# Kernel tuning notes

Hardware: AMD Instinct MI355X
Metric: run time of the kernel (lower is better)

Reference implementation:

```python
import jax, jax.numpy as jnp
import numpy as np

N_NODES = 50000
N_EDGES = 500000
N_GRAPHS = 1024
NF = 128          # node_feature
DIST_DIM = 64
SH_DIM = 64
SH_IN = 9         # spherical_harmonics_l**2, l=3
IN_DIM = 92
N_LAYERS = 5
RBF_BINS = 64
RBF_VMIN, RBF_VMAX = 0.125, 1.4


def _lin(x, W, b):
    return x @ W + b


def setup_inputs() -> dict:
    key = jax.random.key(0)
    ks = jax.random.split(key, 32)
    s = lambda fan_in: 1.0 / np.sqrt(fan_in)

    def W(k, i, o):
        return jax.random.uniform(k, (i, o), jnp.float32, -s(i), s(i))

    inp = {
        "x": jax.random.normal(ks[0], (N_NODES, IN_DIM), jnp.float32),
        "edge_index": jax.random.randint(ks[1], (2, N_EDGES), 0, N_NODES, jnp.int64),
        "sh": jax.random.normal(ks[2], (N_EDGES, SH_IN), jnp.float32),
        "edge_dist": jax.random.uniform(ks[3], (N_EDGES,), jnp.float32, 0.2, 1.0),
        "batch": jnp.sort(jax.random.randint(ks[4], (N_NODES,), 0, N_GRAPHS, jnp.int64)),
        # atom embedding
        "W_emb": W(ks[5], IN_DIM, NF), "b_emb": jnp.zeros((NF,), jnp.float32),
        # sh_mlp: 9 -> 32 -> 64
        "sh_W1": W(ks[6], SH_IN, 32), "sh_b1": jnp.zeros((32,), jnp.float32),
        "sh_W2": W(ks[7], 32, SH_DIM), "sh_b2": jnp.zeros((SH_DIM,), jnp.float32),
        # rbf tail: 64 -> 64 -> 64
        "rbf_W1": W(ks[8], RBF_BINS, 64), "rbf_b1": jnp.zeros((64,), jnp.float32),
        "rbf_W2": W(ks[9], 64, DIST_DIM), "rbf_b2": jnp.zeros((DIST_DIM,), jnp.float32),
        # SFTConv (CGConv-style gated message) stacked over layers: z dim = 3*NF
        "Wg": jnp.stack([W(jax.random.fold_in(ks[10], l), 3 * NF, NF) for l in range(N_LAYERS)]),
        "bg": jnp.zeros((N_LAYERS, NF), jnp.float32),
        "Wc": jnp.stack([W(jax.random.fold_in(ks[11], l), 3 * NF, NF) for l in range(N_LAYERS)]),
        "bc": jnp.zeros((N_LAYERS, NF), jnp.float32),
        # readout fc: 128 -> 128 -> 1
        "fc_W1": W(ks[12], NF, 128), "fc_b1": jnp.zeros((128,), jnp.float32),
        "fc_W2": W(ks[13], 128, 1), "fc_b2": jnp.zeros((1,), jnp.float32),
    }
    return inp


def reference(x, edge_index, sh, edge_dist, batch,
              W_emb, b_emb, sh_W1, sh_b1, sh_W2, sh_b2,
              rbf_W1, rbf_b1, rbf_W2, rbf_b2,
              Wg, bg, Wc, bc, fc_W1, fc_b1, fc_W2, fc_b2):
    # atom embedding: [N, 92] -> [N, 128]
    h = _lin(x, W_emb, b_emb)

    # spherical harmonics edge MLP: [E, 9] -> [E, 64]
    sh_e = _lin(jax.nn.silu(_lin(sh, sh_W1, sh_b1)), sh_W2, sh_b2)

    # RBF expansion of inverse distance (no_grad in torch -> stop_gradient)
    inv_d = jax.lax.stop_gradient(1.0 / edge_dist)[:, None]       # [E, 1]
    centers = jnp.linspace(RBF_VMIN, RBF_VMAX, RBF_BINS, dtype=jnp.float32)
    gamma = 1.0 / (centers[1] - centers[0]) ** 2
    rbf = jnp.exp(-gamma * (inv_d - centers) ** 2)                # [E, 64]
    dist_e = _lin(jax.nn.silu(_lin(rbf, rbf_W1, rbf_b1)), rbf_W2, rbf_b2)

    edge_attr = jnp.concatenate([dist_e, sh_e], axis=-1)          # [E, 128]

    src, dst = edge_index[0], edge_index[1]
    n_nodes = h.shape[0]
    for l in range(Wg.shape[0]):
        # gated CGConv-style message: z = [h_dst, h_src, e]  -> [E, 384]
        z = jnp.concatenate([h[dst], h[src], edge_attr], axis=-1)
        m = jax.nn.sigmoid(z @ Wg[l] + bg[l]) * jax.nn.softplus(z @ Wc[l] + bc[l])
        agg = jax.ops.segment_sum(m, dst, num_segments=n_nodes)   # [N, 128]
        h = h + agg

    # scatter-mean readout over batch ids
    sums = jax.ops.segment_sum(h, batch, num_segments=N_GRAPHS)   # [G, 128]
    counts = jax.ops.segment_sum(jnp.ones((n_nodes,), h.dtype), batch, num_segments=N_GRAPHS)
    pooled = sums / jnp.maximum(counts, 1.0)[:, None]

    out = _lin(jax.nn.silu(_lin(pooled, fc_W1, fc_b1)), fc_W2, fc_b2)  # [G, 1]
    return out.squeeze(-1)
```

## Files before the change

### kernel.cpp

```cpp
#include <hip/hip_runtime.h>

typedef __bf16 bf16x8 __attribute__((ext_vector_type(8)));
typedef __bf16 bf16x4 __attribute__((ext_vector_type(4)));
typedef float  f32x4  __attribute__((ext_vector_type(4)));

#define N_NODES  50000
#define N_EDGES  500000
#define EB       128
#define EP       500096
#define NCH      12
#define N_GRAPHS 1024
#define NF       128
#define IN_DIM   92
#define N_LAYERS 5
#define SPANMAX  256

__device__ __forceinline__ float sigmoidf_(float x) { return 1.0f / (1.0f + __expf(-x)); }
__device__ __forceinline__ float softplusf_(float x) {
    return fmaxf(x, 0.0f) + __logf(1.0f + __expf(-fabsf(x)));
}
__device__ __forceinline__ float siluf_(float x) { return x * sigmoidf_(x); }

__global__ void __launch_bounds__(256) k_fold(const float* __restrict__ Wg,
    const float* __restrict__ Wc, const float* __restrict__ rbW2,
    const float* __restrict__ rbB2, const float* __restrict__ shW2,
    const float* __restrict__ shB2, const float* __restrict__ bg,
    const float* __restrict__ bc, float* __restrict__ Wfold,
    float* __restrict__ bF) {
    int lg = blockIdx.x, l = lg >> 1, g = lg & 1;
    const float* W = (g ? Wc : Wg) + (size_t)l * 384 * 128;
    const float* bsrc = (g ? bc : bg) + l * 128;
    int tid = threadIdx.x;
    for (int idx = tid; idx < 96 * 128; idx += 256) {
        int r = idx >> 7, n = idx & 127;
        float s = 0.f;
        if (r < 64) {
            for (int o = 0; o < 64; ++o) s += rbW2[r * 64 + o] * W[(256 + o) * 128 + n];
        } else {
            int j = r - 64;
            for (int o = 0; o < 64; ++o) s += shW2[j * 64 + o] * W[(320 + o) * 128 + n];
        }
        Wfold[(size_t)lg * 12288 + idx] = s;
    }
    if (tid < 128) {
        float s = bsrc[tid];
        for (int o = 0; o < 64; ++o) s += rbB2[o] * W[(256 + o) * 128 + tid];
        for (int o = 0; o < 64; ++o) s += shB2[o] * W[(320 + o) * 128 + tid];
        bF[lg * 128 + tid] = s;
    }
}

__global__ void __launch_bounds__(256) k_prep_w(const float* __restrict__ Wg,
                                                const float* __restrict__ Wc,
                                                const float* __restrict__ Wfold,
                                                __bf16* __restrict__ WeT,
                                                __bf16* __restrict__ WnT) {
    int t = blockIdx.x * 256 + threadIdx.x;
    if (t >= (240 + 640) * 64) return;
    int frag = t >> 6, lane = t & 63;
    int sub = lane >> 4, mm = lane & 15;
    bf16x8 v;
    if (frag < 240) {
        int lg = frag / 24; int r = frag % 24;
        int m = r / 3; int ks = r % 3;
        #pragma unroll
        for (int j = 0; j < 8; ++j) {
            int k = ks * 32 + sub * 8 + j;
            v[j] = (__bf16)Wfold[(size_t)lg * 12288 + (size_t)k * 128 + m * 16 + mm];
        }
        *(bf16x8*)(WeT + (size_t)frag * 512 + lane * 8) = v;
    } else {
        int f2 = frag - 240;
        int l = f2 / 128; int r = f2 % 128;
        int m = r >> 2; int ks = r & 3;
        int F = m * 16 + mm;
        #pragma unroll
        for (int j = 0; j < 8; ++j) {
            int k = ks * 32 + sub * 8 + j;
            float val;
            if      (F < 128) val = Wg[(size_t)l*384*128 + (size_t)k*128 + F];
            else if (F < 256) val = Wc[(size_t)l*384*128 + (size_t)k*128 + (F-128)];
            else if (F < 384) val = Wg[(size_t)l*384*128 + (size_t)(128+k)*128 + (F-256)];
            else              val = Wc[(size_t)l*384*128 + (size_t)(128+k)*128 + (F-384)];
            v[j] = (__bf16)val;
        }
        *(bf16x8*)(WnT + (size_t)f2 * 512 + lane * 8) = v;
    }
}

__global__ void __launch_bounds__(256) k_deg(const int* __restrict__ dstI,
                                             int* __restrict__ deg) {
    int e = blockIdx.x * 256 + threadIdx.x;
    if (e < N_EDGES) atomicAdd(&deg[dstI[e]], 1);
}

__global__ void __launch_bounds__(1024) k_scan(const int* __restrict__ deg,
                                               int* __restrict__ cursor) {
    __shared__ int ps[1024];
    int t = threadIdx.x;
    const int C = (N_NODES + 1023) / 1024;
    int base = t * C;
    int s = 0;
    for (int i = 0; i < C; ++i) { int idx = base + i; if (idx < N_NODES) s += deg[idx]; }
    ps[t] = s;
    __syncthreads();
    for (int off = 1; off < 1024; off <<= 1) {
        int v = 0;
        if (t >= off) v = ps[t - off];
        __syncthreads();
        if (t >= off) ps[t] += v;
        __syncthreads();
    }
    int run = (t > 0) ? ps[t - 1] : 0;
    for (int i = 0; i < C; ++i) {
        int idx = base + i;
        if (idx < N_NODES) { cursor[idx] = run; run += deg[idx]; }
    }
}

__global__ void __launch_bounds__(256) k_scatter(const int* __restrict__ srcI,
                                                 const int* __restrict__ dstI,
                                                 int* __restrict__ cursor,
                                                 int* __restrict__ perm,
                                                 int* __restrict__ dstS,
                                                 int2* __restrict__ sdS) {
    int e = blockIdx.x * 256 + threadIdx.x;
    if (e >= N_EDGES) return;
    int d = dstI[e];
    int p = atomicAdd(&cursor[d], 1);
    perm[p] = e;
    dstS[p] = d;
    sdS[p] = make_int2(d, srcI[e]);
}

__global__ void __launch_bounds__(128) k_pad(int* __restrict__ dstS,
                                             int2* __restrict__ sdS,
                                             char* __restrict__ ea2) {
    int i = threadIdx.x;
    if (i < EP - N_EDGES) {
        dstS[N_EDGES + i] = N_NODES;
        sdS[N_EDGES + i] = make_int2(N_NODES, 0);
        uint4 z = {0, 0, 0, 0};
        for (int p = 0; p < NCH; ++p)
            *(uint4*)(ea2 + ((size_t)p * EP + N_EDGES + i) * 16) = z;
    }
}

__global__ void __launch_bounds__(256) k_embed(const float* __restrict__ x,
                                               const float* __restrict__ W,
                                               const float* __restrict__ b,
                                               float* __restrict__ h) {
    int tid = threadIdx.x;
    int f = tid & 127;
    int nb = blockIdx.x * 8 + (tid >> 7) * 4;
    const float* x0 = x + (size_t)nb * IN_DIM;
    float a0 = b[f], a1 = a0, a2 = a0, a3 = a0;
    #pragma unroll 4
    for (int k = 0; k < IN_DIM; ++k) {
        float wv = W[k * NF + f];
        a0 = fmaf(x0[k], wv, a0);
        a1 = fmaf(x0[IN_DIM + k], wv, a1);
        a2 = fmaf(x0[2 * IN_DIM + k], wv, a2);
        a3 = fmaf(x0[3 * IN_DIM + k], wv, a3);
    }
    float accs[4] = {a0, a1, a2, a3};
    #pragma unroll
    for (int r = 0; r < 4; ++r)
        h[(size_t)(nb + r) * NF + f] = accs[r];
}

__global__ void __launch_bounds__(256) k_edge(const float* __restrict__ sh,
    const float* __restrict__ dist, const int* __restrict__ perm,
    const float* __restrict__ shW1, const float* __restrict__ shB1,
    const float* __restrict__ rbW1, const float* __restrict__ rbB1,
    char* __restrict__ ea2) {
    __shared__ float wf[4480];
    int tid = threadIdx.x;
    int p = blockIdx.x * 256 + tid;
    bool pv = p < N_EDGES;
    int e = pv ? perm[p] : 0;
    float dv = dist[e];
    float shv[9];
    #pragma unroll
    for (int i = 0; i < 9; ++i) shv[i] = sh[(size_t)e * 9 + i];
    for (int i = tid; i < 288;  i += 256) wf[i]        = shW1[i];
    for (int i = tid; i < 32;   i += 256) wf[288 + i]  = shB1[i];
    for (int i = tid; i < 4096; i += 256) wf[320 + i]  = rbW1[i];
    for (int i = tid; i < 64;   i += 256) wf[4416 + i] = rbB1[i];
    __syncthreads();
    if (!pv) return;

    const float* W1 = wf + 320; const float* B1 = wf + 4416;
    float invd = 1.0f / dv;
    const float step = (1.4f - 0.125f) / 63.0f;
    const float gam = 1.0f / (step * step);
    float hid[64];
    #pragma unroll
    for (int j = 0; j < 64; ++j) hid[j] = B1[j];
    for (int i = 0; i < 64; ++i) {
        float c = 0.125f + i * step;
        float d = invd - c;
        float r = __expf(-gam * d * d);
        #pragma unroll
        for (int j = 0; j < 64; ++j) hid[j] += r * W1[i * 64 + j];
    }
    #pragma unroll
    for (int o8 = 0; o8 < 8; ++o8) {
        bf16x8 v;
        #pragma unroll
        for (int j = 0; j < 8; ++j) v[j] = (__bf16)siluf_(hid[o8 * 8 + j]);
        *(bf16x8*)(ea2 + ((size_t)o8 * EP + p) * 16) = v;
    }
    const float* sW1 = wf; const float* sB1 = wf + 288;
    float h2[32];
    #pragma unroll
    for (int j = 0; j < 32; ++j) h2[j] = sB1[j];
    #pragma unroll
    for (int i = 0; i < 9; ++i) {
        float si = shv[i];
        #pragma unroll
        for (int j = 0; j < 32; ++j) h2[j] += si * sW1[i * 32 + j];
    }
    #pragma unroll
    for (int o8 = 0; o8 < 4; ++o8) {
        bf16x8 v;
        #pragma unroll
        for (int j = 0; j < 8; ++j) v[j] = (__bf16)siluf_(h2[o8 * 8 + j]);
        *(bf16x8*)(ea2 + ((size_t)(8 + o8) * EP + p) * 16) = v;
    }
}

__global__ void __launch_bounds__(256) k_node(const float* __restrict__ h,
                                              const __bf16* __restrict__ WnT,
                                              const float* __restrict__ bgl,
                                              const float* __restrict__ bcl,
                                              __bf16* __restrict__ NBd2,
                                              __bf16* __restrict__ NBs2, int layer) {
    int tid = threadIdx.x, lane = tid & 63, w = tid >> 6;
    int sub = lane >> 4, rA = lane & 15;
    int node0 = blockIdx.x * 32;
    bf16x8 Bf[2][4];
    #pragma unroll
    for (int nt = 0; nt < 2; ++nt)
        #pragma unroll
        for (int ks = 0; ks < 4; ++ks) {
            int node = min(node0 + nt * 16 + rA, N_NODES - 1);
            const float* hr = h + (size_t)node * 128 + ks * 32 + sub * 8;
            f32x4 u0 = *(const f32x4*)hr;
            f32x4 u1 = *(const f32x4*)(hr + 4);
            bf16x8 bv;
            bv[0] = (__bf16)u0[0]; bv[1] = (__bf16)u0[1];
            bv[2] = (__bf16)u0[2]; bv[3] = (__bf16)u0[3];
            bv[4] = (__bf16)u1[0]; bv[5] = (__bf16)u1[1];
            bv[6] = (__bf16)u1[2]; bv[7] = (__bf16)u1[3];
            Bf[nt][ks] = bv;
        }
    const __bf16* Wbase = WnT + (size_t)layer * 128 * 512;
    f32x4 acc[8][2];
    f32x4 zz = {0.f, 0.f, 0.f, 0.f};
    #pragma unroll
    for (int mt = 0; mt < 8; ++mt) { acc[mt][0] = zz; acc[mt][1] = zz; }
    for (int mt = 0; mt < 8; ++mt) {
        int gm = w * 8 + mt;
        bf16x8 Af[4];
        #pragma unroll
        for (int ks = 0; ks < 4; ++ks)
            Af[ks] = *(const bf16x8*)(Wbase + (size_t)(gm * 4 + ks) * 512 + lane * 8);
        #pragma unroll
        for (int nt = 0; nt < 2; ++nt) {
            f32x4 a = acc[mt][nt];
            #pragma unroll
            for (int ks = 0; ks < 4; ++ks)
                a = __builtin_amdgcn_mfma_f32_16x16x32_bf16(Af[ks], Bf[nt][ks], a, 0, 0, 0);
            acc[mt][nt] = a;
        }
    }
    #pragma unroll
    for (int mt = 0; mt < 8; ++mt) {
        int F = (w * 8 + mt) * 16 + sub * 4;
        int part = F >> 7;
        int fq = (F & 127) >> 2;
        f32x4 bias = zz;
        if (part == 0)      bias = *(const f32x4*)(bgl + (F & 127));
        else if (part == 1) bias = *(const f32x4*)(bcl + (F & 127));
        __bf16* buf = (part < 2) ? NBd2 : NBs2;
        int off = fq * 8 + (part & 1) * 4;
        #pragma unroll
        for (int nt = 0; nt < 2; ++nt) {
            int node = node0 + nt * 16 + rA;
            if (node >= N_NODES) continue;
            f32x4 vv = acc[mt][nt];
            vv[0] += bias[0]; vv[1] += bias[1]; vv[2] += bias[2]; vv[3] += bias[3];
            bf16x4 bv;
            bv[0] = (__bf16)vv[0]; bv[1] = (__bf16)vv[1];
            bv[2] = (__bf16)vv[2]; bv[3] = (__bf16)vv[3];
            *(bf16x4*)(buf + (size_t)node * 256 + off) = bv;
        }
    }
}

__global__ void __launch_bounds__(512) k_msg(
    const char* __restrict__ ea2, const int* __restrict__ dstS,
    const int2* __restrict__ sdS, const __bf16* __restrict__ WeT,
    const __bf16* __restrict__ NBd2, const __bf16* __restrict__ NBs2,
    float* __restrict__ h, int layer)
{
    __shared__ __align__(16) float mF[EB * 128];
    __shared__ int rs[SPANMAX], re[SPANMAX];
    int tid = threadIdx.x, lane = tid & 63, w = tid >> 6;
    int sub = lane >> 4, rA = lane & 15;
    int e0 = blockIdx.x * EB;
    int fq = w * 4 + sub;
    int n0 = dstS[e0];

    if (tid < EB) {
        int d = dstS[e0 + tid];
        int di = min(d - n0, SPANMAX - 1);
        if (tid == 0 || dstS[e0 + tid - 1] != d) {
            rs[di] = tid;
            if (tid > 0) {
                int dp = dstS[e0 + tid - 1];
                for (int g = dp + 1; g < d && (g - n0) < SPANMAX; ++g) {
                    rs[g - n0] = 0; re[g - n0] = 0;
                }
            }
        }
        if (tid == EB - 1 || dstS[e0 + tid + 1] != d) re[di] = tid + 1;
    }

    bf16x8 Ag[3], Ac[3];
    {
        const __bf16* bg_ = WeT + (size_t)(((layer * 2 + 0) * 8 + w) * 3) * 512;
        const __bf16* bc_ = WeT + (size_t)(((layer * 2 + 1) * 8 + w) * 3) * 512;
        #pragma unroll
        for (int ks = 0; ks < 3; ++ks) {
            Ag[ks] = *(const bf16x8*)(bg_ + ks * 512 + lane * 8);
            Ac[ks] = *(const bf16x8*)(bc_ + ks * 512 + lane * 8);
        }
    }

    const char* eb0 = ea2 + ((size_t)(0 + sub) * EP + e0 + rA) * 16;
    const char* eb1 = ea2 + ((size_t)(4 + sub) * EP + e0 + rA) * 16;
    const char* eb2 = ea2 + ((size_t)(8 + sub) * EP + e0 + rA) * 16;
    const int2* sdp = sdS + e0 + rA;
    char* mfp = (char*)mF + rA * 512 + ((w * 64 + sub * 16) ^ ((rA & 7) << 4));

    f32x4 zz = {0.f, 0.f, 0.f, 0.f};
    bf16x8 bfr[2][3];
    bf16x8 dv[2], sv[2];

    {
        int2 sd = sdp[0];
        int dstc = min(sd.x, N_NODES - 1);
        bfr[0][0] = *(const bf16x8*)(eb0);
        bfr[0][1] = *(const bf16x8*)(eb1);
        bfr[0][2] = *(const bf16x8*)(eb2);
        dv[0] = *(const bf16x8*)(NBd2 + (size_t)dstc * 256 + fq * 8);
        sv[0] = *(const bf16x8*)(NBs2 + (size_t)sd.y * 256 + fq * 8);
    }
    #pragma unroll
    for (int nt = 0; nt < EB / 16; ++nt) {
        int cur = nt & 1, nxt = cur ^ 1;
        if (nt + 1 < EB / 16) {
            int2 sd = sdp[(nt + 1) * 16];
            int dstc = min(sd.x, N_NODES - 1);
            bfr[nxt][0] = *(const bf16x8*)(eb0 + (nt + 1) * 256);
            bfr[nxt][1] = *(const bf16x8*)(eb1 + (nt + 1) * 256);
            bfr[nxt][2] = *(const bf16x8*)(eb2 + (nt + 1) * 256);
            dv[nxt] = *(const bf16x8*)(NBd2 + (size_t)dstc * 256 + fq * 8);
            sv[nxt] = *(const bf16x8*)(NBs2 + (size_t)sd.y * 256 + fq * 8);
        }
        f32x4 aG = zz, aC = zz;
        #pragma unroll
        for (int ks = 0; ks < 3; ++ks) {
            aG = __builtin_amdgcn_mfma_f32_16x16x32_bf16(Ag[ks], bfr[cur][ks], aG, 0, 0, 0);
            aC = __builtin_amdgcn_mfma_f32_16x16x32_bf16(Ac[ks], bfr[cur][ks], aC, 0, 0, 0);
        }
        f32x4 mv;
        #pragma unroll
        for (int r = 0; r < 4; ++r) {
            float gi = aG[r] + (float)dv[cur][r] + (float)sv[cur][r];
            float ci = aC[r] + (float)dv[cur][4 + r] + (float)sv[cur][4 + r];
            mv[r] = sigmoidf_(gi) * softplusf_(ci);
        }
        *(f32x4*)(mfp + nt * 8192) = mv;
    }
    __syncthreads();
    int span = min(dstS[e0 + EB - 1] - n0 + 1, SPANMAX);
    int items = span * 32;
    for (int it = tid; it < items; it += 512) {
        int ln = it >> 5, fqq = it & 31;
        int rs_ = rs[ln], re_ = re[ln];
        f32x4 s = zz;
        for (int e = rs_; e < re_; ++e) {
            f32x4 v = *(const f32x4*)((char*)mF + e * 512 + ((fqq * 16) ^ ((e & 7) << 4)));
            s[0] += v[0]; s[1] += v[1]; s[2] += v[2]; s[3] += v[3];
        }
        int node = n0 + ln;
        float* dp = h + (size_t)node * 128 + fqq * 4;
        if (ln == 0 || ln == span - 1) {
            atomicAdd(dp + 0, s[0]); atomicAdd(dp + 1, s[1]);
            atomicAdd(dp + 2, s[2]); atomicAdd(dp + 3, s[3]);
        } else {
            dp[0] += s[0]; dp[1] += s[1]; dp[2] += s[2]; dp[3] += s[3];
        }
    }
}

__global__ void __launch_bounds__(128) k_readout(const float* __restrict__ h,
    const int* __restrict__ batch, const float* __restrict__ W1,
    const float* __restrict__ b1, const float* __restrict__ W2,
    const float* __restrict__ b2, float* __restrict__ out) {
    int g = blockIdx.x, tid = threadIdx.x;
    __shared__ int se[2];
    __shared__ float pl[NF];
    __shared__ float red[2];
    if (tid < 2) {
        int target = g + tid;
        int lo = 0, hi = N_NODES;
        while (lo < hi) { int mid = (lo + hi) >> 1; if (batch[mid] < target) lo = mid + 1; else hi = mid; }
        se[tid] = lo;
    }
    __syncthreads();
    int s = se[0], e = se[1];
    float sum = 0.0f;
    for (int n = s; n < e; ++n) sum += h[(size_t)n * NF + tid];
    float cnt = (float)max(e - s, 1);
    pl[tid] = sum / cnt;
    __syncthreads();
    float acc = b1[tid];
    for (int c = 0; c < NF; ++c) acc += pl[c] * W1[c * NF + tid];
    float hid = siluf_(acc);
    float v = hid * W2[tid];
    #pragma unroll
    for (int off = 32; off > 0; off >>= 1) v += __shfl_down(v, off);
    if ((tid & 63) == 0) red[tid >> 6] = v;
    __syncthreads();
    if (tid == 0) out[g] = red[0] + red[1] + b2[0];
}

extern "C" void kernel_launch(void* const* d_in, const int* in_sizes, int n_in,
                              void* d_out, int out_size, void* d_ws, size_t ws_size,
                              hipStream_t stream) {
    const float* x     = (const float*)d_in[0];
    const int*   eidx  = (const int*)d_in[1];
    const float* sh    = (const float*)d_in[2];
    const float* edist = (const float*)d_in[3];
    const int*   batch = (const int*)d_in[4];
    const float* W_emb = (const float*)d_in[5];
    const float* b_emb = (const float*)d_in[6];
    const float* shW1  = (const float*)d_in[7];
    const float* shB1  = (const float*)d_in[8];
    const float* shW2  = (const float*)d_in[9];
    const float* shB2  = (const float*)d_in[10];
    const float* rbW1  = (const float*)d_in[11];
    const float* rbB1  = (const float*)d_in[12];
    const float* rbW2  = (const float*)d_in[13];
    const float* rbB2  = (const float*)d_in[14];
    const float* Wg    = (const float*)d_in[15];
    const float* bg    = (const float*)d_in[16];
    const float* Wc    = (const float*)d_in[17];
    const float* bc    = (const float*)d_in[18];
    const float* fcW1  = (const float*)d_in[19];
    const float* fcb1  = (const float*)d_in[20];
    const float* fcW2  = (const float*)d_in[21];
    const float* fcb2  = (const float*)d_in[22];
    const int* srcI = eidx;
    const int* dstI = eidx + N_EDGES;

    char* ws = (char*)d_ws;
    float*  h     = (float*)(ws + 0);
    char*   ea2   = (char*)(ws + 25600512);
    int*    dstS  = (int*)(ws + 121618944);
    int2*   sdS   = (int2*)(ws + 123619328);
    int*    deg   = (int*)(ws + 127620096);
    int*    curs  = (int*)(ws + 127820096);
    int*    perm  = (int*)(ws + 128020096);
    __bf16* WeT   = (__bf16*)(ws + 130020096);
    __bf16* WnT   = (__bf16*)(ws + 130265856);
    float*  Wfold = (float*)(ws + 130921216);
    float*  bF    = (float*)(ws + 131412736);
    __bf16* NBd2  = (__bf16*)(ws + 131417856);
    __bf16* NBs2  = (__bf16*)(ws + 157017856);

    hipMemsetAsync(deg, 0, (size_t)N_NODES * sizeof(int), stream);
    k_fold<<<10, 256, 0, stream>>>(Wg, Wc, rbW2, rbB2, shW2, shB2, bg, bc, Wfold, bF);
    k_prep_w<<<220, 256, 0, stream>>>(Wg, Wc, Wfold, WeT, WnT);
    k_embed<<<N_NODES / 8, 256, 0, stream>>>(x, W_emb, b_emb, h);
    k_deg<<<(N_EDGES + 255) / 256, 256, 0, stream>>>(dstI, deg);
    k_scan<<<1, 1024, 0, stream>>>(deg, curs);
    k_scatter<<<(N_EDGES + 255) / 256, 256, 0, stream>>>(srcI, dstI, curs, perm, dstS, sdS);
    k_edge<<<(N_EDGES + 255) / 256, 256, 0, stream>>>(sh, edist, perm, shW1, shB1,
                                                      rbW1, rbB1, ea2);
    k_pad<<<1, 128, 0, stream>>>(dstS, sdS, ea2);
    for (int l = 0; l < N_LAYERS; ++l) {
        const float* bgF = bF + (l * 2 + 0) * 128;
        const float* bcF = bF + (l * 2 + 1) * 128;
        k_node<<<(N_NODES + 31) / 32, 256, 0, stream>>>(h, WnT, bgF, bcF, NBd2, NBs2, l);
        k_msg<<<EP / EB, 512, 0, stream>>>(ea2, dstS, sdS, WeT, NBd2, NBs2, h, l);
    }
    k_readout<<<N_GRAPHS, 128, 0, stream>>>(h, batch, fcW1, fcb1, fcW2, fcb2, (float*)d_out);
}
```

Measured before the change: 1.158 ms.

## Parallelize weight folding, pre-permute edge inputs in scatter, prescale node offsets

```diff
diff --git a/kernel.cpp b/kernel.cpp
--- a/kernel.cpp
+++ b/kernel.cpp
@@ -27,26 +27,25 @@
     const float* __restrict__ shB2, const float* __restrict__ bg,
     const float* __restrict__ bc, float* __restrict__ Wfold,
     float* __restrict__ bF) {
-    int lg = blockIdx.x, l = lg >> 1, g = lg & 1;
+    int lg = blockIdx.x / 48, chunk = blockIdx.x % 48;
+    int l = lg >> 1, g = lg & 1;
     const float* W = (g ? Wc : Wg) + (size_t)l * 384 * 128;
-    const float* bsrc = (g ? bc : bg) + l * 128;
-    int tid = threadIdx.x;
-    for (int idx = tid; idx < 96 * 128; idx += 256) {
-        int r = idx >> 7, n = idx & 127;
-        float s = 0.f;
-        if (r < 64) {
-            for (int o = 0; o < 64; ++o) s += rbW2[r * 64 + o] * W[(256 + o) * 128 + n];
-        } else {
-            int j = r - 64;
-            for (int o = 0; o < 64; ++o) s += shW2[j * 64 + o] * W[(320 + o) * 128 + n];
-        }
-        Wfold[(size_t)lg * 12288 + idx] = s;
-    }
-    if (tid < 128) {
-        float s = bsrc[tid];
-        for (int o = 0; o < 64; ++o) s += rbB2[o] * W[(256 + o) * 128 + tid];
-        for (int o = 0; o < 64; ++o) s += shB2[o] * W[(320 + o) * 128 + tid];
-        bF[lg * 128 + tid] = s;
+    int idx = chunk * 256 + threadIdx.x;
+    int r = idx >> 7, n = idx & 127;
+    float s = 0.f;
+    if (r < 64) {
+        for (int o = 0; o < 64; ++o) s += rbW2[r * 64 + o] * W[(256 + o) * 128 + n];
+    } else {
+        int j = r - 64;
+        for (int o = 0; o < 64; ++o) s += shW2[j * 64 + o] * W[(320 + o) * 128 + n];
+    }
+    Wfold[(size_t)lg * 12288 + idx] = s;
+    if (chunk == 0 && threadIdx.x < 128) {
+        const float* bsrc = (g ? bc : bg) + l * 128;
+        float b = bsrc[threadIdx.x];
+        for (int o = 0; o < 64; ++o) b += rbB2[o] * W[(256 + o) * 128 + threadIdx.x];
+        for (int o = 0; o < 64; ++o) b += shB2[o] * W[(320 + o) * 128 + threadIdx.x];
+        bF[lg * 128 + threadIdx.x] = b;
     }
 }
 
@@ -120,17 +119,22 @@
 
 __global__ void __launch_bounds__(256) k_scatter(const int* __restrict__ srcI,
                                                  const int* __restrict__ dstI,
+                                                 const float* __restrict__ edist,
+                                                 const float* __restrict__ sh,
                                                  int* __restrict__ cursor,
-                                                 int* __restrict__ perm,
                                                  int* __restrict__ dstS,
-                                                 int2* __restrict__ sdS) {
+                                                 int2* __restrict__ sdS,
+                                                 float* __restrict__ distS,
+                                                 float* __restrict__ shS) {
     int e = blockIdx.x * 256 + threadIdx.x;
     if (e >= N_EDGES) return;
     int d = dstI[e];
     int p = atomicAdd(&cursor[d], 1);
-    perm[p] = e;
     dstS[p] = d;
-    sdS[p] = make_int2(d, srcI[e]);
+    sdS[p] = make_int2(d * 256, srcI[e] * 256);
+    distS[p] = edist[e];
+    #pragma unroll
+    for (int i = 0; i < 9; ++i) shS[(size_t)p * 9 + i] = sh[(size_t)e * 9 + i];
 }
 
 __global__ void __launch_bounds__(128) k_pad(int* __restrict__ dstS,
@@ -139,7 +143,7 @@
     int i = threadIdx.x;
     if (i < EP - N_EDGES) {
         dstS[N_EDGES + i] = N_NODES;
-        sdS[N_EDGES + i] = make_int2(N_NODES, 0);
+        sdS[N_EDGES + i] = make_int2((N_NODES - 1) * 256, 0);
         uint4 z = {0, 0, 0, 0};
         for (int p = 0; p < NCH; ++p)
             *(uint4*)(ea2 + ((size_t)p * EP + N_EDGES + i) * 16) = z;
@@ -169,8 +173,8 @@
         h[(size_t)(nb + r) * NF + f] = accs[r];
 }
 
-__global__ void __launch_bounds__(256) k_edge(const float* __restrict__ sh,
-    const float* __restrict__ dist, const int* __restrict__ perm,
+__global__ void __launch_bounds__(256) k_edge(const float* __restrict__ distS,
+    const float* __restrict__ shS,
     const float* __restrict__ shW1, const float* __restrict__ shB1,
     const float* __restrict__ rbW1, const float* __restrict__ rbB1,
     char* __restrict__ ea2) {
@@ -178,11 +182,11 @@
     int tid = threadIdx.x;
     int p = blockIdx.x * 256 + tid;
     bool pv = p < N_EDGES;
-    int e = pv ? perm[p] : 0;
-    float dv = dist[e];
+    int pc = pv ? p : 0;
+    float dv = distS[pc];
     float shv[9];
     #pragma unroll
-    for (int i = 0; i < 9; ++i) shv[i] = sh[(size_t)e * 9 + i];
+    for (int i = 0; i < 9; ++i) shv[i] = shS[(size_t)pc * 9 + i];
     for (int i = tid; i < 288;  i += 256) wf[i]        = shW1[i];
     for (int i = tid; i < 32;   i += 256) wf[288 + i]  = shB1[i];
     for (int i = tid; i < 4096; i += 256) wf[320 + i]  = rbW1[i];
@@ -343,6 +347,8 @@
     const char* eb1 = ea2 + ((size_t)(4 + sub) * EP + e0 + rA) * 16;
     const char* eb2 = ea2 + ((size_t)(8 + sub) * EP + e0 + rA) * 16;
     const int2* sdp = sdS + e0 + rA;
+    const __bf16* nbd = NBd2 + fq * 8;
+    const __bf16* nbs = NBs2 + fq * 8;
     char* mfp = (char*)mF + rA * 512 + ((w * 64 + sub * 16) ^ ((rA & 7) << 4));
 
     f32x4 zz = {0.f, 0.f, 0.f, 0.f};
@@ -351,24 +357,22 @@
 
     {
         int2 sd = sdp[0];
-        int dstc = min(sd.x, N_NODES - 1);
         bfr[0][0] = *(const bf16x8*)(eb0);
         bfr[0][1] = *(const bf16x8*)(eb1);
         bfr[0][2] = *(const bf16x8*)(eb2);
-        dv[0] = *(const bf16x8*)(NBd2 + (size_t)dstc * 256 + fq * 8);
-        sv[0] = *(const bf16x8*)(NBs2 + (size_t)sd.y * 256 + fq * 8);
+        dv[0] = *(const bf16x8*)(nbd + sd.x);
+        sv[0] = *(const bf16x8*)(nbs + sd.y);
     }
     #pragma unroll
     for (int nt = 0; nt < EB / 16; ++nt) {
         int cur = nt & 1, nxt = cur ^ 1;
         if (nt + 1 < EB / 16) {
             int2 sd = sdp[(nt + 1) * 16];
-            int dstc = min(sd.x, N_NODES - 1);
             bfr[nxt][0] = *(const bf16x8*)(eb0 + (nt + 1) * 256);
             bfr[nxt][1] = *(const bf16x8*)(eb1 + (nt + 1) * 256);
             bfr[nxt][2] = *(const bf16x8*)(eb2 + (nt + 1) * 256);
-            dv[nxt] = *(const bf16x8*)(NBd2 + (size_t)dstc * 256 + fq * 8);
-            sv[nxt] = *(const bf16x8*)(NBs2 + (size_t)sd.y * 256 + fq * 8);
+            dv[nxt] = *(const bf16x8*)(nbd + sd.x);
+            sv[nxt] = *(const bf16x8*)(nbs + sd.y);
         }
         f32x4 aG = zz, aC = zz;
         #pragma unroll
@@ -475,22 +479,24 @@
     int2*   sdS   = (int2*)(ws + 123619328);
     int*    deg   = (int*)(ws + 127620096);
     int*    curs  = (int*)(ws + 127820096);
-    int*    perm  = (int*)(ws + 128020096);
-    __bf16* WeT   = (__bf16*)(ws + 130020096);
-    __bf16* WnT   = (__bf16*)(ws + 130265856);
-    float*  Wfold = (float*)(ws + 130921216);
-    float*  bF    = (float*)(ws + 131412736);
-    __bf16* NBd2  = (__bf16*)(ws + 131417856);
-    __bf16* NBs2  = (__bf16*)(ws + 157017856);
+    float*  distS = (float*)(ws + 128020096);
+    float*  shS   = (float*)(ws + 130020480);
+    __bf16* WeT   = (__bf16*)(ws + 148023936);
+    __bf16* WnT   = (__bf16*)(ws + 148269696);
+    float*  Wfold = (float*)(ws + 148925056);
+    float*  bF    = (float*)(ws + 149416576);
+    __bf16* NBd2  = (__bf16*)(ws + 149421696);
+    __bf16* NBs2  = (__bf16*)(ws + 175021696);
 
     hipMemsetAsync(deg, 0, (size_t)N_NODES * sizeof(int), stream);
-    k_fold<<<10, 256, 0, stream>>>(Wg, Wc, rbW2, rbB2, shW2, shB2, bg, bc, Wfold, bF);
+    k_fold<<<480, 256, 0, stream>>>(Wg, Wc, rbW2, rbB2, shW2, shB2, bg, bc, Wfold, bF);
     k_prep_w<<<220, 256, 0, stream>>>(Wg, Wc, Wfold, WeT, WnT);
     k_embed<<<N_NODES / 8, 256, 0, stream>>>(x, W_emb, b_emb, h);
     k_deg<<<(N_EDGES + 255) / 256, 256, 0, stream>>>(dstI, deg);
     k_scan<<<1, 1024, 0, stream>>>(deg, curs);
-    k_scatter<<<(N_EDGES + 255) / 256, 256, 0, stream>>>(srcI, dstI, curs, perm, dstS, sdS);
-    k_edge<<<(N_EDGES + 255) / 256, 256, 0, stream>>>(sh, edist, perm, shW1, shB1,
+    k_scatter<<<(N_EDGES + 255) / 256, 256, 0, stream>>>(srcI, dstI, edist, sh, curs,
+                                                         dstS, sdS, distS, shS);
+    k_edge<<<(N_EDGES + 255) / 256, 256, 0, stream>>>(distS, shS, shW1, shB1,
                                                       rbW1, rbB1, ea2);
     k_pad<<<1, 128, 0, stream>>>(dstS, sdS, ea2);
     for (int l = 0; l < N_LAYERS; ++l) {
```

Result: faster. 1.072 ms (median of 2 runs) (-7.4%).
